# Optimization experiments

Measured on AMD Instinct MI355X. Metric: run time of the kernel, lower is better.

Reference implementation:

```python
import jax, jax.numpy as jnp
import numpy as np

EMBEDDING_DIM = 256
CODEBOOK_SIZE = 1024
COMMITMENT_COST = 0.25


def setup_inputs() -> dict:
    key = jax.random.key(0)
    k1, k2 = jax.random.split(key)
    inputs = jax.random.normal(k1, (16, 4096, EMBEDDING_DIM), dtype=jnp.float32)
    embeddings = jax.random.normal(k2, (EMBEDDING_DIM, CODEBOOK_SIZE), dtype=jnp.float32)
    return {"inputs": inputs, "embeddings": embeddings}


def reference(inputs, embeddings):
    # inputs: [B, T, D]; embeddings: [D, K]
    D = embeddings.shape[0]
    K = embeddings.shape[1]
    flat = inputs.reshape(-1, D)  # [N, D]

    sim = flat @ embeddings
    dists = (jnp.sum(flat * flat, axis=1, keepdims=True)
             + jnp.sum(embeddings * embeddings, axis=0)
             - 2.0 * sim)
    flat_idx = jnp.argmin(dists, axis=1)  # [N]

    encodings = jax.nn.one_hot(flat_idx, K, dtype=jnp.float32)  # [N, K]
    encoding_indices = flat_idx.reshape(inputs.shape[:-1])  # [B, T]

    # embedding lookup: gather rows of embeddings^T -> [B, T, D]
    quantized = jnp.take(embeddings.T, encoding_indices, axis=0)

    e_latent_loss = jnp.mean(jnp.square(jax.lax.stop_gradient(quantized) - inputs))
    q_latent_loss = jnp.mean(jnp.square(quantized - jax.lax.stop_gradient(inputs)))
    loss = q_latent_loss + COMMITMENT_COST * e_latent_loss

    # straight-through estimator
    quantized_st = inputs + jax.lax.stop_gradient(quantized - inputs)

    return quantized_st, encodings, encoding_indices, loss
```

## Files before the change

kernel.cpp:

```cpp
#include <hip/hip_runtime.h>

#define N_ROWS 65536
#define DIM    256
#define KCB    1024

#define Q_OFF    0
#define ENC_OFF  (N_ROWS * DIM)
#define IDX_OFF  (ENC_OFF + N_ROWS * KCB)
#define LOSS_OFF (IDX_OFF + N_ROWS)

#define ET_OFF   (ENC_OFF + 0)
#define NRM_OFF  (ENC_OFF + 262144)
#define IDXI_OFF (ENC_OFF + 263168)
#define PART_OFF (ENC_OFF + 328704)
#define AMB_OFF  (ENC_OFF + 345088)
#define PMIN_OFF (ENC_OFF + 524288)
#define A2_OFF   (ENC_OFF + 4718592)
#define BST_OFF  (ENC_OFF + 21495808)

#define TAU 0.05f
#define MAXCAND 20000
#define MAXFB   16000

typedef short  bf16x8 __attribute__((ext_vector_type(8)));
typedef float  f32x4  __attribute__((ext_vector_type(4)));
typedef unsigned short u16x8 __attribute__((ext_vector_type(8)));
#define AS1 __attribute__((address_space(1)))
#define AS3 __attribute__((address_space(3)))

__device__ inline unsigned short f2bf(float x) {
    unsigned u = __float_as_uint(x);
    return (unsigned short)((u + 0x7FFFu + ((u >> 16) & 1u)) >> 16);
}
__device__ inline float bf2f(unsigned short b) {
    return __uint_as_float(((unsigned)b) << 16);
}

__global__ __launch_bounds__(256)
void vq_prep_a(const float* __restrict__ X, float* __restrict__ out) {
    unsigned short* A2 = (unsigned short*)(out + A2_OFF);
    int gid = blockIdx.x * 256 + threadIdx.x;
    int row = gid >> 5;
    int d0  = (gid & 31) * 8;
    const float* xp = X + (size_t)row * DIM + d0;
    float4 v0 = *(const float4*)xp;
    float4 v1 = *(const float4*)(xp + 4);
    float xv[8] = {v0.x, v0.y, v0.z, v0.w, v1.x, v1.y, v1.z, v1.w};
    u16x8 h, l;
#pragma unroll
    for (int i = 0; i < 8; ++i) {
        unsigned short hb = f2bf(xv[i]);
        h[i] = hb;
        l[i] = f2bf(xv[i] - bf2f(hb));
    }
    *(u16x8*)(A2 + (size_t)row * 512 + d0) = h;
    *(u16x8*)(A2 + (size_t)row * 512 + 256 + d0) = l;
}

__global__ __launch_bounds__(64)
void vq_prep_b(const float* __restrict__ E, float* __restrict__ out) {
    float* ET  = out + ET_OFF;
    float* nrm = out + NRM_OFF;
    unsigned short* B2 = (unsigned short*)(out + BST_OFF);
    const int k = blockIdx.x, t = threadIdx.x;
    float v[4]; float s = 0.f;
    ushort4 hb, lb;
#pragma unroll
    for (int i = 0; i < 4; ++i) {
        float e = E[(size_t)(t * 4 + i) * KCB + k];
        v[i] = e; s += e * e;
        unsigned short h = f2bf(e);
        ((unsigned short*)&hb)[i] = h;
        ((unsigned short*)&lb)[i] = f2bf(e - bf2f(h));
    }
    *(float4*)(ET + (size_t)k * DIM + t * 4) = *(float4*)v;
    *(ushort4*)(B2 + (size_t)k * 512 + t * 4) = hb;
    *(ushort4*)(B2 + (size_t)k * 512 + 256 + t * 4) = lb;
#pragma unroll
    for (int off = 32; off >= 1; off >>= 1) s += __shfl_xor(s, off);
    if (t == 0) nrm[k] = s;
    if (k == 0 && t == 0) { int* a = (int*)(out + AMB_OFF); a[0] = 0; a[1] = 0; }
}

__global__ __launch_bounds__(256, 3)
void vq_gemm(float* __restrict__ out) {
    __shared__ short lds[24576];
    const unsigned short* A2 = (const unsigned short*)(out + A2_OFF);
    const unsigned short* B2 = (const unsigned short*)(out + BST_OFF);
    const float* nrm = out + NRM_OFF;
    float4* pmin = (float4*)(out + PMIN_OFF);

    const int orig = blockIdx.x;
    const int mapped = (orig & 7) * 512 + (orig >> 3);
    const int rb = mapped >> 3, cb = mapped & 7;
    const int row0 = rb * 128, col0 = cb * 128;

    const int tid = threadIdx.x;
    const int lane = tid & 63, l15 = lane & 15, lhi = lane >> 4;
    const int w = tid >> 6, wr = w >> 1, wc = w & 1;
    const int swz = (l15 & 7) * 8;

    f32x4 acc[4][4];
#pragma unroll
    for (int i = 0; i < 4; ++i)
#pragma unroll
        for (int j = 0; j < 4; ++j) acc[i][j] = (f32x4){0.f, 0.f, 0.f, 0.f};

    const int sr   = tid >> 3;
    const int sksw = ((tid & 7) ^ ((tid >> 3) & 7)) * 8;
    const int wofs = (tid & 192) * 16;

#define STAGE4(SRC, R0, KOFF, LDSB)                                           \
    _Pragma("unroll")                                                         \
    for (int i = 0; i < 4; ++i) {                                             \
        __builtin_amdgcn_global_load_lds(                                     \
            (const AS1 unsigned*)((SRC) + (size_t)((R0) + i * 32 + sr) * 512  \
                                  + (KOFF) + sksw),                           \
            (AS3 unsigned*)((char*)lds + (LDSB) + i * 4096 + wofs), 16, 0, 0);\
    }

    for (int kr = 0; kr < 4; ++kr) {
        __syncthreads();
        STAGE4(A2, row0, kr * 64, 0);
        STAGE4(B2, col0, kr * 64, 16384);
        STAGE4(B2, col0, 256 + kr * 64, 32768);
        asm volatile("s_waitcnt vmcnt(0)" ::: "memory");
        __syncthreads();
#pragma unroll
        for (int kk = 0; kk < 2; ++kk) {
            const int cofs = (kk * 32 + lhi * 8) ^ swz;
            bf16x8 af[4], bh[4], bl[4];
#pragma unroll
            for (int mi = 0; mi < 4; ++mi)
                af[mi] = *(const bf16x8*)&lds[(wr * 64 + mi * 16 + l15) * 64 + cofs];
#pragma unroll
            for (int ni = 0; ni < 4; ++ni) {
                bh[ni] = *(const bf16x8*)&lds[8192 + (wc * 64 + ni * 16 + l15) * 64 + cofs];
                bl[ni] = *(const bf16x8*)&lds[16384 + (wc * 64 + ni * 16 + l15) * 64 + cofs];
            }
#pragma unroll
            for (int mi = 0; mi < 4; ++mi)
#pragma unroll
                for (int ni = 0; ni < 4; ++ni)
                    acc[mi][ni] = __builtin_amdgcn_mfma_f32_16x16x32_bf16(
                        af[mi], bh[ni], acc[mi][ni], 0, 0, 0);
#pragma unroll
            for (int mi = 0; mi < 4; ++mi)
#pragma unroll
                for (int ni = 0; ni < 4; ++ni)
                    acc[mi][ni] = __builtin_amdgcn_mfma_f32_16x16x32_bf16(
                        af[mi], bl[ni], acc[mi][ni], 0, 0, 0);
        }
    }
    for (int kr = 0; kr < 4; ++kr) {
        __syncthreads();
        STAGE4(A2, row0, 256 + kr * 64, 0);
        STAGE4(B2, col0, kr * 64, 16384);
        asm volatile("s_waitcnt vmcnt(0)" ::: "memory");
        __syncthreads();
#pragma unroll
        for (int kk = 0; kk < 2; ++kk) {
            const int cofs = (kk * 32 + lhi * 8) ^ swz;
            bf16x8 af[4], bh[4];
#pragma unroll
            for (int mi = 0; mi < 4; ++mi)
                af[mi] = *(const bf16x8*)&lds[(wr * 64 + mi * 16 + l15) * 64 + cofs];
#pragma unroll
            for (int ni = 0; ni < 4; ++ni)
                bh[ni] = *(const bf16x8*)&lds[8192 + (wc * 64 + ni * 16 + l15) * 64 + cofs];
#pragma unroll
            for (int mi = 0; mi < 4; ++mi)
#pragma unroll
                for (int ni = 0; ni < 4; ++ni)
                    acc[mi][ni] = __builtin_amdgcn_mfma_f32_16x16x32_bf16(
                        af[mi], bh[ni], acc[mi][ni], 0, 0, 0);
        }
    }
#undef STAGE4

    float nv[4];
#pragma unroll
    for (int ni = 0; ni < 4; ++ni) nv[ni] = nrm[col0 + wc * 64 + ni * 16 + l15];
#pragma unroll
    for (int mi = 0; mi < 4; ++mi)
#pragma unroll
        for (int j = 0; j < 4; ++j) {
            float a = 3.4e38f, b = 3.4e38f; int ia = 0;
#pragma unroll
            for (int ni = 0; ni < 4; ++ni) {
                float dist = fmaf(-2.f, acc[mi][ni][j], nv[ni]);
                int col = col0 + wc * 64 + ni * 16 + l15;
                if (dist < a) { b = a; a = dist; ia = col; }
                else if (dist < b) b = dist;
            }
#pragma unroll
            for (int off = 1; off < 16; off <<= 1) {
                float oa = __shfl_xor(a, off);
                float ob = __shfl_xor(b, off);
                int   oi = __shfl_xor(ia, off);
                if (oa < a || (oa == a && oi < ia)) { b = fminf(a, ob); a = oa; ia = oi; }
                else b = fminf(b, oa);
            }
            if (l15 == 0) {
                int grow = row0 + wr * 64 + mi * 16 + lhi * 4 + j;
                float4 pv;
                pv.x = a; pv.y = __int_as_float(ia); pv.z = b; pv.w = 0.f;
                pmin[(size_t)grow * 16 + cb * 2 + wc] = pv;
            }
        }
}

__global__ __launch_bounds__(256)
void vq_combine(float* __restrict__ out) {
    const float4* pmin = (const float4*)(out + PMIN_OFF);
    int* idxi = (int*)(out + IDXI_OFF);
    int* amb  = (int*)(out + AMB_OFF);
    int* fb   = (int*)(out + PART_OFF);
    const int row = blockIdx.x * 256 + threadIdx.x;
    float a = 3.4e38f, b = 3.4e38f; int ia = 0;
#pragma unroll
    for (int s = 0; s < 16; ++s) {
        float4 p = pmin[(size_t)row * 16 + s];
        float v1 = p.x; int i1 = __float_as_int(p.y);
        if (v1 < a || (v1 == a && i1 < ia)) { b = fminf(a, p.z); a = v1; ia = i1; }
        else b = fminf(b, v1);
    }
    idxi[row] = ia;
    if (b - a < TAU) {
        const float lim = a + TAU;
        int cands[6]; int nc = 0; bool ok = true;
#pragma unroll
        for (int s = 0; s < 16; ++s) {
            float4 p = pmin[(size_t)row * 16 + s];
            if (p.z < lim) ok = false;
            if (p.x < lim) { if (nc < 6) cands[nc] = __float_as_int(p.y); ++nc; }
        }
        if (ok && nc <= 6) {
            int pos = atomicAdd(&amb[0], 1);
            if (pos < MAXCAND) {
                int* e = amb + 16 + pos * 8;
                e[0] = row; e[1] = nc;
#pragma unroll
                for (int c = 0; c < 6; ++c) e[2 + c] = (c < nc) ? cands[c] : 0;
            } else ok = false;
        } else ok = false;
        if (!ok) {
            int pos = atomicAdd(&amb[1], 1);
            if (pos < MAXFB) fb[pos] = row;
        }
    }
}

__global__ __launch_bounds__(256)
void vq_rescore_cand(const float* __restrict__ X, float* __restrict__ out) {
    const float* ET  = out + ET_OFF;
    const float* nrm = out + NRM_OFF;
    const int* amb = (const int*)(out + AMB_OFF);
    int* idxi = (int*)(out + IDXI_OFF);
    int count = amb[0]; if (count > MAXCAND) count = MAXCAND;
    for (int it = blockIdx.x * 256 + threadIdx.x; it < count; it += gridDim.x * 256) {
        const int* e = amb + 16 + it * 8;
        const int row = e[0], nc = e[1];
        const float* xp = X + (size_t)row * DIM;
        float best = 3.4e38f; int bi = 0x7fffffff;
        for (int c = 0; c < nc; ++c) {
            const int code = e[2 + c];
            const float* ep = ET + (size_t)code * DIM;
            float acc = 0.f;
#pragma unroll 8
            for (int d = 0; d < 256; ++d)
                acc = fmaf(xp[d], ep[d], acc);
            float dist = fmaf(-2.f, acc, nrm[code]);
            if (dist < best || (dist == best && code < bi)) { best = dist; bi = code; }
        }
        idxi[row] = bi;
    }
}

__global__ __launch_bounds__(256)
void vq_rescore_fb(const float* __restrict__ X, float* __restrict__ out) {
    __shared__ float xs[4][256];
    const float* ET  = out + ET_OFF;
    const float* nrm = out + NRM_OFF;
    const int* amb = (const int*)(out + AMB_OFF);
    const int* fb  = (const int*)(out + PART_OFF);
    int* idxi = (int*)(out + IDXI_OFF);
    const int wid = threadIdx.x >> 6, lane = threadIdx.x & 63;
    int count = amb[1]; if (count > MAXFB) count = MAXFB;
    for (int it = blockIdx.x * 4 + wid; it < count; it += gridDim.x * 4) {
        const int row = fb[it];
        *(float4*)&xs[wid][lane * 4] = *(const float4*)(X + (size_t)row * DIM + lane * 4);
        float best = 3.4e38f; int bi = 0;
        for (int cc = 0; cc < 16; ++cc) {
            const int code = cc * 64 + lane;
            const float* ep = ET + (size_t)code * DIM;
            float acc = 0.f;
#pragma unroll
            for (int d = 0; d < 256; d += 4) {
                float4 ev = *(const float4*)(ep + d);
                acc = fmaf(xs[wid][d],     ev.x, acc);
                acc = fmaf(xs[wid][d + 1], ev.y, acc);
                acc = fmaf(xs[wid][d + 2], ev.z, acc);
                acc = fmaf(xs[wid][d + 3], ev.w, acc);
            }
            float dist = fmaf(-2.f, acc, nrm[code]);
            if (dist < best) { best = dist; bi = code; }
        }
#pragma unroll
        for (int off = 1; off < 64; off <<= 1) {
            float ov = __shfl_xor(best, off);
            int   oi = __shfl_xor(bi, off);
            if (ov < best || (ov == best && oi < bi)) { best = ov; bi = oi; }
        }
        if (lane == 0) idxi[row] = bi;
    }
}

__global__ __launch_bounds__(256)
void vq_outputs(const float* __restrict__ X, float* __restrict__ out) {
    const float* ET  = out + ET_OFF;
    const int*   idx = (const int*)(out + IDXI_OFF);
    float*       part = out + PART_OFF;
    __shared__ float red[4];
    const int row  = blockIdx.x * 4 + (threadIdx.x >> 6);
    const int lane = threadIdx.x & 63;
    const int id   = idx[row];
    float4 e = *(const float4*)(ET + (size_t)id * DIM + lane * 4);
    float4 x = *(const float4*)(X + (size_t)row * DIM + lane * 4);
    float dx = e.x - x.x, dy = e.y - x.y, dz = e.z - x.z, dw = e.w - x.w;
    float4 q;
    q.x = x.x + dx; q.y = x.y + dy; q.z = x.z + dz; q.w = x.w + dw;
    *(float4*)(out + Q_OFF + (size_t)row * DIM + lane * 4) = q;
    float s = dx * dx + dy * dy + dz * dz + dw * dw;
#pragma unroll
    for (int off = 32; off >= 1; off >>= 1) s += __shfl_xor(s, off);
    if (lane == 0) {
        red[threadIdx.x >> 6] = s;
        out[IDX_OFF + row] = (float)id;
    }
    __syncthreads();
    if (threadIdx.x == 0) part[blockIdx.x] = red[0] + red[1] + red[2] + red[3];
}

__global__ __launch_bounds__(256)
void vq_loss(float* __restrict__ out) {
    const float* part = out + PART_OFF;
    __shared__ double red[256];
    const int tid = threadIdx.x;
    double s = 0.0;
    for (int i = tid; i < 16384; i += 256) s += (double)part[i];
    red[tid] = s;
    __syncthreads();
    for (int off = 128; off > 0; off >>= 1) {
        if (tid < off) red[tid] += red[tid + off];
        __syncthreads();
    }
    if (tid == 0)
        out[LOSS_OFF] = (float)(1.25 * red[0] / (double)((size_t)N_ROWS * DIM));
}

__global__ __launch_bounds__(256)
void vq_encodings(float* __restrict__ out) {
    const float* idxf = out + IDX_OFF;
    float4* enc4 = (float4*)(out + ENC_OFF);
    const size_t total4 = (size_t)N_ROWS * KCB / 4;
    const size_t stride = (size_t)gridDim.x * blockDim.x;
    for (size_t g = (size_t)blockIdx.x * blockDim.x + threadIdx.x; g < total4; g += stride) {
        int n  = (int)(g >> 8);
        int c0 = ((int)g & 255) * 4;
        int r  = (int)idxf[n] - c0;
        float4 v;
        v.x = (r == 0) ? 1.f : 0.f;
        v.y = (r == 1) ? 1.f : 0.f;
        v.z = (r == 2) ? 1.f : 0.f;
        v.w = (r == 3) ? 1.f : 0.f;
        enc4[g] = v;
    }
}

extern "C" void kernel_launch(void* const* d_in, const int* in_sizes, int n_in,
                              void* d_out, int out_size, void* d_ws, size_t ws_size,
                              hipStream_t stream) {
    const float* X = (const float*)d_in[0];
    const float* E = (const float*)d_in[1];
    float* out = (float*)d_out;

    vq_prep_a      <<<8192, 256, 0, stream>>>(X, out);
    vq_prep_b      <<<1024,  64, 0, stream>>>(E, out);
    vq_gemm        <<<4096, 256, 0, stream>>>(out);
    vq_combine     <<<256,  256, 0, stream>>>(out);
    vq_rescore_cand<<<256,  256, 0, stream>>>(X, out);
    vq_rescore_fb  <<<128,  256, 0, stream>>>(X, out);
    vq_outputs     <<<16384, 256, 0, stream>>>(X, out);
    vq_loss        <<<1,    256, 0, stream>>>(out);
    vq_encodings   <<<2048, 256, 0, stream>>>(out);
}
```

Before: 733.6 us.

## Fuse prep, combine/rescore, and loss/encodings kernels to cut launches

Merges the two prep kernels into one launch, folds the combine, candidate rescore and fallback rescore into a single resolve kernel, and merges the loss reduction into the encodings kernel. Ambiguous rows are now rescored in place, and fallback rows are kept in a per-block shared list instead of global atomic queues. This removes four kernel launches and the global candidate and fallback buffers. The cost is that a block with many fallback rows serialises their full 1024-code rescans on its four waves, and candidate rescoring now runs divergently per thread inside the combine pass.

```diff
diff --git a/kernel.cpp b/kernel.cpp
--- a/kernel.cpp
+++ b/kernel.cpp
@@ -13,14 +13,11 @@
 #define NRM_OFF  (ENC_OFF + 262144)
 #define IDXI_OFF (ENC_OFF + 263168)
 #define PART_OFF (ENC_OFF + 328704)
-#define AMB_OFF  (ENC_OFF + 345088)
 #define PMIN_OFF (ENC_OFF + 524288)
 #define A2_OFF   (ENC_OFF + 4718592)
 #define BST_OFF  (ENC_OFF + 21495808)
 
 #define TAU 0.05f
-#define MAXCAND 20000
-#define MAXFB   16000
 
 typedef short  bf16x8 __attribute__((ext_vector_type(8)));
 typedef float  f32x4  __attribute__((ext_vector_type(4)));
@@ -37,49 +34,50 @@
 }
 
 __global__ __launch_bounds__(256)
-void vq_prep_a(const float* __restrict__ X, float* __restrict__ out) {
-    unsigned short* A2 = (unsigned short*)(out + A2_OFF);
-    int gid = blockIdx.x * 256 + threadIdx.x;
-    int row = gid >> 5;
-    int d0  = (gid & 31) * 8;
-    const float* xp = X + (size_t)row * DIM + d0;
-    float4 v0 = *(const float4*)xp;
-    float4 v1 = *(const float4*)(xp + 4);
-    float xv[8] = {v0.x, v0.y, v0.z, v0.w, v1.x, v1.y, v1.z, v1.w};
-    u16x8 h, l;
-#pragma unroll
-    for (int i = 0; i < 8; ++i) {
-        unsigned short hb = f2bf(xv[i]);
-        h[i] = hb;
-        l[i] = f2bf(xv[i] - bf2f(hb));
-    }
-    *(u16x8*)(A2 + (size_t)row * 512 + d0) = h;
-    *(u16x8*)(A2 + (size_t)row * 512 + 256 + d0) = l;
-}
-
-__global__ __launch_bounds__(64)
-void vq_prep_b(const float* __restrict__ E, float* __restrict__ out) {
-    float* ET  = out + ET_OFF;
-    float* nrm = out + NRM_OFF;
-    unsigned short* B2 = (unsigned short*)(out + BST_OFF);
-    const int k = blockIdx.x, t = threadIdx.x;
-    float v[4]; float s = 0.f;
-    ushort4 hb, lb;
-#pragma unroll
-    for (int i = 0; i < 4; ++i) {
-        float e = E[(size_t)(t * 4 + i) * KCB + k];
-        v[i] = e; s += e * e;
-        unsigned short h = f2bf(e);
-        ((unsigned short*)&hb)[i] = h;
-        ((unsigned short*)&lb)[i] = f2bf(e - bf2f(h));
-    }
-    *(float4*)(ET + (size_t)k * DIM + t * 4) = *(float4*)v;
-    *(ushort4*)(B2 + (size_t)k * 512 + t * 4) = hb;
-    *(ushort4*)(B2 + (size_t)k * 512 + 256 + t * 4) = lb;
-#pragma unroll
-    for (int off = 32; off >= 1; off >>= 1) s += __shfl_xor(s, off);
-    if (t == 0) nrm[k] = s;
-    if (k == 0 && t == 0) { int* a = (int*)(out + AMB_OFF); a[0] = 0; a[1] = 0; }
+void vq_prep(const float* __restrict__ X, const float* __restrict__ E,
+             float* __restrict__ out) {
+    if (blockIdx.x < 8192) {
+        unsigned short* A2 = (unsigned short*)(out + A2_OFF);
+        int gid = blockIdx.x * 256 + threadIdx.x;
+        int row = gid >> 5;
+        int d0  = (gid & 31) * 8;
+        const float* xp = X + (size_t)row * DIM + d0;
+        float4 v0 = *(const float4*)xp;
+        float4 v1 = *(const float4*)(xp + 4);
+        float xv[8] = {v0.x, v0.y, v0.z, v0.w, v1.x, v1.y, v1.z, v1.w};
+        u16x8 h, l;
+#pragma unroll
+        for (int i = 0; i < 8; ++i) {
+            unsigned short hb = f2bf(xv[i]);
+            h[i] = hb;
+            l[i] = f2bf(xv[i] - bf2f(hb));
+        }
+        *(u16x8*)(A2 + (size_t)row * 512 + d0) = h;
+        *(u16x8*)(A2 + (size_t)row * 512 + 256 + d0) = l;
+    } else {
+        const int k = blockIdx.x - 8192, t = threadIdx.x;
+        if (t < 64) {
+            float* ET  = out + ET_OFF;
+            float* nrm = out + NRM_OFF;
+            unsigned short* B2 = (unsigned short*)(out + BST_OFF);
+            float v[4]; float s = 0.f;
+            ushort4 hb, lb;
+#pragma unroll
+            for (int i = 0; i < 4; ++i) {
+                float e = E[(size_t)(t * 4 + i) * KCB + k];
+                v[i] = e; s += e * e;
+                unsigned short h = f2bf(e);
+                ((unsigned short*)&hb)[i] = h;
+                ((unsigned short*)&lb)[i] = f2bf(e - bf2f(h));
+            }
+            *(float4*)(ET + (size_t)k * DIM + t * 4) = *(float4*)v;
+            *(ushort4*)(B2 + (size_t)k * 512 + t * 4) = hb;
+            *(ushort4*)(B2 + (size_t)k * 512 + 256 + t * 4) = lb;
+#pragma unroll
+            for (int off = 32; off >= 1; off >>= 1) s += __shfl_xor(s, off);
+            if (t == 0) nrm[k] = s;
+        }
+    }
 }
 
 __global__ __launch_bounds__(256, 3)
@@ -211,12 +209,19 @@
 }
 
 __global__ __launch_bounds__(256)
-void vq_combine(float* __restrict__ out) {
+void vq_resolve(const float* __restrict__ X, float* __restrict__ out) {
+    __shared__ int   fb_list[256];
+    __shared__ int   fb_cnt;
+    __shared__ float xs[4][256];
     const float4* pmin = (const float4*)(out + PMIN_OFF);
+    const float*  ET   = out + ET_OFF;
+    const float*  nrm  = out + NRM_OFF;
     int* idxi = (int*)(out + IDXI_OFF);
-    int* amb  = (int*)(out + AMB_OFF);
-    int* fb   = (int*)(out + PART_OFF);
-    const int row = blockIdx.x * 256 + threadIdx.x;
+    const int tid = threadIdx.x;
+    if (tid == 0) fb_cnt = 0;
+    __syncthreads();
+
+    const int row = blockIdx.x * 256 + tid;
     float a = 3.4e38f, b = 3.4e38f; int ia = 0;
 #pragma unroll
     for (int s = 0; s < 16; ++s) {
@@ -225,7 +230,7 @@
         if (v1 < a || (v1 == a && i1 < ia)) { b = fminf(a, p.z); a = v1; ia = i1; }
         else b = fminf(b, v1);
     }
-    idxi[row] = ia;
+    int result = ia;
     if (b - a < TAU) {
         const float lim = a + TAU;
         int cands[6]; int nc = 0; bool ok = true;
@@ -236,60 +241,32 @@
             if (p.x < lim) { if (nc < 6) cands[nc] = __float_as_int(p.y); ++nc; }
         }
         if (ok && nc <= 6) {
-            int pos = atomicAdd(&amb[0], 1);
-            if (pos < MAXCAND) {
-                int* e = amb + 16 + pos * 8;
-                e[0] = row; e[1] = nc;
-#pragma unroll
-                for (int c = 0; c < 6; ++c) e[2 + c] = (c < nc) ? cands[c] : 0;
-            } else ok = false;
-        } else ok = false;
-        if (!ok) {
-            int pos = atomicAdd(&amb[1], 1);
-            if (pos < MAXFB) fb[pos] = row;
-        }
-    }
-}
-
-__global__ __launch_bounds__(256)
-void vq_rescore_cand(const float* __restrict__ X, float* __restrict__ out) {
-    const float* ET  = out + ET_OFF;
-    const float* nrm = out + NRM_OFF;
-    const int* amb = (const int*)(out + AMB_OFF);
-    int* idxi = (int*)(out + IDXI_OFF);
-    int count = amb[0]; if (count > MAXCAND) count = MAXCAND;
-    for (int it = blockIdx.x * 256 + threadIdx.x; it < count; it += gridDim.x * 256) {
-        const int* e = amb + 16 + it * 8;
-        const int row = e[0], nc = e[1];
-        const float* xp = X + (size_t)row * DIM;
-        float best = 3.4e38f; int bi = 0x7fffffff;
-        for (int c = 0; c < nc; ++c) {
-            const int code = e[2 + c];
-            const float* ep = ET + (size_t)code * DIM;
-            float acc = 0.f;
+            const float* xp = X + (size_t)row * DIM;
+            float best = 3.4e38f; int bi = 0x7fffffff;
+            for (int c = 0; c < nc; ++c) {
+                const int code = cands[c];
+                const float* ep = ET + (size_t)code * DIM;
+                float acc = 0.f;
 #pragma unroll 8
-            for (int d = 0; d < 256; ++d)
-                acc = fmaf(xp[d], ep[d], acc);
-            float dist = fmaf(-2.f, acc, nrm[code]);
-            if (dist < best || (dist == best && code < bi)) { best = dist; bi = code; }
-        }
-        idxi[row] = bi;
-    }
-}
-
-__global__ __launch_bounds__(256)
-void vq_rescore_fb(const float* __restrict__ X, float* __restrict__ out) {
-    __shared__ float xs[4][256];
-    const float* ET  = out + ET_OFF;
-    const float* nrm = out + NRM_OFF;
-    const int* amb = (const int*)(out + AMB_OFF);
-    const int* fb  = (const int*)(out + PART_OFF);
-    int* idxi = (int*)(out + IDXI_OFF);
-    const int wid = threadIdx.x >> 6, lane = threadIdx.x & 63;
-    int count = amb[1]; if (count > MAXFB) count = MAXFB;
-    for (int it = blockIdx.x * 4 + wid; it < count; it += gridDim.x * 4) {
-        const int row = fb[it];
-        *(float4*)&xs[wid][lane * 4] = *(const float4*)(X + (size_t)row * DIM + lane * 4);
+                for (int d = 0; d < 256; ++d)
+                    acc = fmaf(xp[d], ep[d], acc);
+                float dist = fmaf(-2.f, acc, nrm[code]);
+                if (dist < best || (dist == best && code < bi)) { best = dist; bi = code; }
+            }
+            result = bi;
+        } else {
+            int pos = atomicAdd(&fb_cnt, 1);
+            fb_list[pos] = row;
+        }
+    }
+    idxi[row] = result;
+    __syncthreads();
+
+    const int wid = tid >> 6, lane = tid & 63;
+    const int fbc = fb_cnt;
+    for (int i = wid; i < fbc; i += 4) {
+        const int row2 = fb_list[i];
+        *(float4*)&xs[wid][lane * 4] = *(const float4*)(X + (size_t)row2 * DIM + lane * 4);
         float best = 3.4e38f; int bi = 0;
         for (int cc = 0; cc < 16; ++cc) {
             const int code = cc * 64 + lane;
@@ -312,7 +289,7 @@
             int   oi = __shfl_xor(bi, off);
             if (ov < best || (ov == best && oi < bi)) { best = ov; bi = oi; }
         }
-        if (lane == 0) idxi[row] = bi;
+        if (lane == 0) idxi[row2] = bi;
     }
 }
 
@@ -343,24 +320,23 @@
 }
 
 __global__ __launch_bounds__(256)
-void vq_loss(float* __restrict__ out) {
-    const float* part = out + PART_OFF;
-    __shared__ double red[256];
-    const int tid = threadIdx.x;
-    double s = 0.0;
-    for (int i = tid; i < 16384; i += 256) s += (double)part[i];
-    red[tid] = s;
-    __syncthreads();
-    for (int off = 128; off > 0; off >>= 1) {
-        if (tid < off) red[tid] += red[tid + off];
-        __syncthreads();
-    }
-    if (tid == 0)
-        out[LOSS_OFF] = (float)(1.25 * red[0] / (double)((size_t)N_ROWS * DIM));
-}
-
-__global__ __launch_bounds__(256)
-void vq_encodings(float* __restrict__ out) {
+void vq_encloss(float* __restrict__ out) {
+    if (blockIdx.x == 0) {
+        const float* part = out + PART_OFF;
+        __shared__ double red[256];
+        const int tid = threadIdx.x;
+        double s = 0.0;
+        for (int i = tid; i < 16384; i += 256) s += (double)part[i];
+        red[tid] = s;
+        __syncthreads();
+        for (int off = 128; off > 0; off >>= 1) {
+            if (tid < off) red[tid] += red[tid + off];
+            __syncthreads();
+        }
+        if (tid == 0)
+            out[LOSS_OFF] = (float)(1.25 * red[0] / (double)((size_t)N_ROWS * DIM));
+        __syncthreads();
+    }
     const float* idxf = out + IDX_OFF;
     float4* enc4 = (float4*)(out + ENC_OFF);
     const size_t total4 = (size_t)N_ROWS * KCB / 4;
@@ -385,13 +361,9 @@
     const float* E = (const float*)d_in[1];
     float* out = (float*)d_out;
 
-    vq_prep_a      <<<8192, 256, 0, stream>>>(X, out);
-    vq_prep_b      <<<1024,  64, 0, stream>>>(E, out);
-    vq_gemm        <<<4096, 256, 0, stream>>>(out);
-    vq_combine     <<<256,  256, 0, stream>>>(out);
-    vq_rescore_cand<<<256,  256, 0, stream>>>(X, out);
-    vq_rescore_fb  <<<128,  256, 0, stream>>>(X, out);
-    vq_outputs     <<<16384, 256, 0, stream>>>(X, out);
-    vq_loss        <<<1,    256, 0, stream>>>(out);
-    vq_encodings   <<<2048, 256, 0, stream>>>(out);
-}
+    vq_prep    <<<9216,  256, 0, stream>>>(X, E, out);
+    vq_gemm    <<<4096,  256, 0, stream>>>(out);
+    vq_resolve <<<256,   256, 0, stream>>>(X, out);
+    vq_outputs <<<16384, 256, 0, stream>>>(X, out);
+    vq_encloss <<<2048,  256, 0, stream>>>(out);
+}
```

Result: faster. 677.1 us (-7.7%).
